# Kernel optimization log

Measured on AMD Instinct MI355X. Metric: run time of the kernel, lower is better.

## Reference

```python
import jax, jax.numpy as jnp
import numpy as np

DIM = 768; HEADS = 12; HD = DIM // HEADS; WS = 8; MLP = 4 * DIM; AH = DIM // 4
SCALE = HD ** -0.5
ADAPT_SCALE = 0.5  # self.scale in AdapterBlock3D (standard SAM-adapter constant)

def _ln(x, g, b, eps=1e-5):
    m = x.mean(-1, keepdims=True)
    v = ((x - m) ** 2).mean(-1, keepdims=True)
    return (x - m) * jax.lax.rsqrt(v + eps) * g + b

def _gelu(x):
    return jax.nn.gelu(x, approximate=False)  # torch nn.GELU default = exact erf

def _win_partition(x, ws):
    B, D, H, W, C = x.shape
    pd = (ws - D % ws) % ws; ph = (ws - H % ws) % ws; pw = (ws - W % ws) % ws
    if pd or ph or pw:
        x = jnp.pad(x, ((0, 0), (0, pd), (0, ph), (0, pw), (0, 0)))
    Dp, Hp, Wp = D + pd, H + ph, W + pw
    x = x.reshape(B, Dp // ws, ws, Hp // ws, ws, Wp // ws, ws, C)
    win = x.transpose(0, 1, 3, 5, 2, 4, 6, 7).reshape(-1, ws, ws, ws, C)
    return win, (Dp, Hp, Wp)

def _win_unpartition(win, ws, pad_dhw, dhw):
    Dp, Hp, Wp = pad_dhw; D, H, W = dhw
    B = win.shape[0] // (Dp * Hp * Wp // ws ** 3)
    x = win.reshape(B, Dp // ws, Hp // ws, Wp // ws, ws, ws, ws, -1)
    x = x.transpose(0, 1, 4, 2, 5, 3, 6, 7).reshape(B, Dp, Hp, Wp, -1)
    return x[:, :D, :H, :W, :]

def _rel(rel_pos, size):
    # q_size == k_size == size, rel_pos has 2*size-1 rows -> pure gather
    idx = jnp.arange(size)[:, None] - jnp.arange(size)[None, :] + (size - 1)
    return rel_pos[idx]  # (size, size, HD)

def _attention(x, qkv_w, qkv_b, rpd, rph, rpw, proj_w, proj_b):
    Bw = x.shape[0]; N = WS ** 3
    qkv = (x.reshape(Bw, N, DIM) @ qkv_w.T + qkv_b).reshape(Bw, N, 3, HEADS, HD)
    qkv = qkv.transpose(2, 0, 3, 1, 4).reshape(3, Bw * HEADS, N, HD)
    q, k, v = qkv[0], qkv[1], qkv[2]
    attn = jnp.einsum('bqc,bkc->bqk', q * SCALE, k)  # (Bw*H, N, N)
    rq = q.reshape(-1, WS, WS, WS, HD)
    rel_d = jnp.einsum('bdhwc,dkc->bdhwk', rq, _rel(rpd, WS))
    rel_h = jnp.einsum('bdhwc,hkc->bdhwk', rq, _rel(rph, WS))
    rel_w = jnp.einsum('bdhwc,wkc->bdhwk', rq, _rel(rpw, WS))
    attn = (attn.reshape(-1, WS, WS, WS, WS, WS, WS)
            + rel_d[:, :, :, :, :, None, None]
            + rel_h[:, :, :, :, None, :, None]
            + rel_w[:, :, :, :, None, None, :]).reshape(-1, N, N)
    attn = jax.nn.softmax(attn, axis=-1)
    out = jnp.einsum('bqk,bkc->bqc', attn, v).reshape(Bw, HEADS, WS, WS, WS, HD)
    out = out.transpose(0, 2, 3, 4, 1, 5).reshape(Bw, WS, WS, WS, DIM)
    return out @ proj_w.T + proj_b

def _adapter(x, w1, b1, w2, b2, skip):
    xs = _gelu(x @ w1.T + b1) @ w2.T + b2
    return x + xs if skip else xs

def setup_inputs() -> dict:
    key = jax.random.key(0)
    ks = jax.random.split(key, 24)
    r = lambda k, s: jax.random.normal(k, s, dtype=jnp.float32) * 0.02
    return {
        'x': jax.random.normal(ks[0], (2, 16, 16, 16, DIM), dtype=jnp.float32),
        'ln1_g': jnp.ones((DIM,), jnp.float32), 'ln1_b': jnp.zeros((DIM,), jnp.float32),
        'qkv_w': r(ks[1], (3 * DIM, DIM)), 'qkv_b': r(ks[2], (3 * DIM,)),
        'rel_pos_d': r(ks[3], (2 * WS - 1, HD)),
        'rel_pos_h': r(ks[4], (2 * WS - 1, HD)),
        'rel_pos_w': r(ks[5], (2 * WS - 1, HD)),
        'proj_w': r(ks[6], (DIM, DIM)), 'proj_b': r(ks[7], (DIM,)),
        'aa1_w': r(ks[8], (AH, DIM)), 'aa1_b': r(ks[9], (AH,)),
        'aa2_w': r(ks[10], (DIM, AH)), 'aa2_b': r(ks[11], (DIM,)),
        'ln2_g': jnp.ones((DIM,), jnp.float32), 'ln2_b': jnp.zeros((DIM,), jnp.float32),
        'mlp1_w': r(ks[12], (MLP, DIM)), 'mlp1_b': r(ks[13], (MLP,)),
        'mlp2_w': r(ks[14], (DIM, MLP)), 'mlp2_b': r(ks[15], (DIM,)),
        'ma1_w': r(ks[16], (AH, DIM)), 'ma1_b': r(ks[17], (AH,)),
        'ma2_w': r(ks[18], (DIM, AH)), 'ma2_b': r(ks[19], (DIM,)),
    }

def reference(x, ln1_g, ln1_b, qkv_w, qkv_b, rel_pos_d, rel_pos_h, rel_pos_w,
              proj_w, proj_b, aa1_w, aa1_b, aa2_w, aa2_b, ln2_g, ln2_b,
              mlp1_w, mlp1_b, mlp2_w, mlp2_b, ma1_w, ma1_b, ma2_w, ma2_b):
    B, D, H, W, C = x.shape
    shortcut = x
    h = _ln(x, ln1_g, ln1_b)
    h, pad_dhw = _win_partition(h, WS)
    h = _attention(h, qkv_w, qkv_b, rel_pos_d, rel_pos_h, rel_pos_w, proj_w, proj_b)
    h = _adapter(h, aa1_w, aa1_b, aa2_w, aa2_b, skip=True)  # Attention_Adapter
    h = _win_unpartition(h, WS, pad_dhw, (D, H, W))
    h = shortcut + h
    hn = _ln(h, ln2_g, ln2_b)
    mlp_out = _gelu(hn @ mlp1_w.T + mlp1_b) @ mlp2_w.T + mlp2_b
    adapt_out = _adapter(hn, ma1_w, ma1_b, ma2_w, ma2_b, skip=False)  # MLP_Adapter
    return h + mlp_out + ADAPT_SCALE * adapt_out
```

## Files before the change

kernel.cpp:

```cpp
#include <hip/hip_runtime.h>

typedef unsigned short u16;
typedef __attribute__((ext_vector_type(4))) float f32x4;
typedef __attribute__((ext_vector_type(8))) short s16x8;

#define TOK 8192
#define NDIM 768
#define NHEADS 12
#define WHN 192
#define WHSZ 32768
#define L2E 1.4426950408889634f
#define SCL2 (0.125f * L2E)

#if __has_builtin(__builtin_amdgcn_exp2f)
#define EXP2F __builtin_amdgcn_exp2f
#else
#define EXP2F exp2f
#endif

__device__ __forceinline__ u16 f2bf(float f) {
  union { float f; unsigned u; } x; x.f = f;
  unsigned r = x.u + 0x7fffu + ((x.u >> 16) & 1u);
  return (u16)(r >> 16);
}
__device__ __forceinline__ float bf2f(u16 u) {
  union { unsigned u; float f; } x; x.u = ((unsigned)u) << 16;
  return x.f;
}
__device__ __forceinline__ float gelu_f(float v) {
  float z = fabsf(v) * 0.70710678118654752f;
  float t = __builtin_amdgcn_rcpf(1.0f + 0.3275911f * z);
  float poly = t * (0.254829592f +
               t * (-0.284496736f +
               t * (1.421413741f +
               t * (-1.453152027f + t * 1.061405429f))));
  float erfv = 1.0f - poly * __expf(-z * z);
  erfv = copysignf(erfv, v);
  return 0.5f * v * (1.0f + erfv);
}
__device__ __forceinline__ f32x4 mfma16(s16x8 a, s16x8 b, f32x4 c) {
  return __builtin_amdgcn_mfma_f32_16x16x32_bf16(a, b, c, 0, 0, 0);
}
__device__ __forceinline__ void glds16(const u16* g, u16* l) {
  __builtin_amdgcn_global_load_lds(
      (const __attribute__((address_space(1))) unsigned int*)g,
      (__attribute__((address_space(3))) unsigned int*)l, 16, 0, 0);
}
template<int N> __device__ __forceinline__ void waitvm() {
  if constexpr (N == 0)      asm volatile("s_waitcnt vmcnt(0)" ::: "memory");
  else if constexpr (N == 2) asm volatile("s_waitcnt vmcnt(2)" ::: "memory");
  else if constexpr (N == 3) asm volatile("s_waitcnt vmcnt(3)" ::: "memory");
  else if constexpr (N == 4) asm volatile("s_waitcnt vmcnt(4)" ::: "memory");
  else if constexpr (N == 6) asm volatile("s_waitcnt vmcnt(6)" ::: "memory");
  __builtin_amdgcn_sched_barrier(0);
}
__device__ __forceinline__ int tok_of(int wi, int n) {
  int b = wi >> 3;
  int d = (((wi >> 2) & 1) << 3) | (n >> 6);
  int h = (((wi >> 1) & 1) << 3) | ((n >> 3) & 7);
  int w = ((wi & 1) << 3) | (n & 7);
  return (b << 12) | (d << 8) | (h << 4) | w;
}

struct WConv {
  const float* src[11];
  u16* dst[11];
  int n[11];
};
__global__ __launch_bounds__(256) void conv_weights(WConv a) {
  int stride = gridDim.x * blockDim.x;
  int t0 = blockIdx.x * blockDim.x + threadIdx.x;
  for (int s = 0; s < 11; s++) {
    const float4* src = (const float4*)a.src[s];
    u16* dst = a.dst[s];
    int n4 = a.n[s] >> 2;
    for (int i = t0; i < n4; i += stride) {
      float4 v = src[i];
      ushort4 o;
      o.x = f2bf(v.x); o.y = f2bf(v.y); o.z = f2bf(v.z); o.w = f2bf(v.w);
      *(ushort4*)(dst + 4 * (size_t)i) = o;
    }
  }
}

__global__ __launch_bounds__(256) void ln_bf16(const float* __restrict__ in,
    const float* __restrict__ gamma, const float* __restrict__ beta,
    u16* __restrict__ out) {
  const int row = blockIdx.x;
  const int tid = threadIdx.x;
  const float* xr = in + (size_t)row * NDIM;
  float v0 = xr[tid], v1 = xr[tid + 256], v2 = xr[tid + 512];
  float s = v0 + v1 + v2;
  float q = v0 * v0 + v1 * v1 + v2 * v2;
  for (int o = 32; o; o >>= 1) { s += __shfl_down(s, o); q += __shfl_down(q, o); }
  __shared__ float ss[4], sq[4];
  int wave = tid >> 6, lane = tid & 63;
  if (lane == 0) { ss[wave] = s; sq[wave] = q; }
  __syncthreads();
  s = ss[0] + ss[1] + ss[2] + ss[3];
  q = sq[0] + sq[1] + sq[2] + sq[3];
  float mean = s * (1.0f / 768.0f);
  float var = q * (1.0f / 768.0f) - mean * mean;
  float rstd = rsqrtf(var + 1e-5f);
  u16* orow = out + (size_t)row * NDIM;
  float v[3] = {v0, v1, v2};
  #pragma unroll
  for (int i = 0; i < 3; i++) {
    int c = tid + i * 256;
    orow[c] = f2bf((v[i] - mean) * rstd * gamma[c] + beta[c]);
  }
}

template<int BM, int BN, int TPB, int EPI>
__global__ __launch_bounds__(TPB) void gemm_bf16(
    const u16* __restrict__ A, const u16* __restrict__ W,
    const float* __restrict__ bias, int M, int N, int K,
    u16* __restrict__ obf, float* __restrict__ of,
    const float* __restrict__ add1, const float* __restrict__ add2) {
  constexpr int BK = 32;
  constexpr int WCOLS = TPB / 128;
  constexpr int WM = BM / 2, WN = BN / WCOLS;
  constexpr int MF = WM / 16, NF = WN / 16;
  constexpr int ACH = BM * BK / (8 * TPB);
  constexpr int BCH = BN * BK / (8 * TPB);
  constexpr int LPT = ACH + BCH;
  __shared__ __align__(16) u16 As[3][BM * BK];
  __shared__ __align__(16) u16 Bs[3][BN * BK];
  const int bm = blockIdx.x, bn = blockIdx.y;
  const int tid = threadIdx.x;
  const int wave = tid >> 6, lane = tid & 63;
  const int wr = wave / WCOLS, wc = wave % WCOLS;
  const int g = lane >> 4, c15 = lane & 15;
  f32x4 acc[MF][NF] = {};
  const u16* Ab = A + (size_t)(bm * BM) * K;
  const u16* Wb = W + (size_t)(bn * BN) * K;
  auto stage = [&](int k0, int b) {
    #pragma unroll
    for (int i = 0; i < ACH; i++) {
      int L = i * TPB + tid;
      glds16(Ab + (size_t)(L >> 2) * K + k0 + (((L & 3) ^ ((L >> 2) & 3)) * 8),
             &As[b][L * 8]);
    }
    #pragma unroll
    for (int i = 0; i < BCH; i++) {
      int L = i * TPB + tid;
      glds16(Wb + (size_t)(L >> 2) * K + k0 + (((L & 3) ^ ((L >> 2) & 3)) * 8),
             &Bs[b][L * 8]);
    }
  };
  const int NT = K / BK;
  stage(0, 0);
  stage(BK, 1);
  for (int t = 0; t < NT; t++) {
    int buf = t % 3;
    if (t < NT - 1) waitvm<LPT>(); else waitvm<0>();
    __builtin_amdgcn_s_barrier();
    __builtin_amdgcn_sched_barrier(0);
    if (t + 2 < NT) stage((t + 2) * BK, (t + 2) % 3);
    s16x8 af[MF], bfr[NF];
    #pragma unroll
    for (int mi = 0; mi < MF; mi++) {
      int r = wr * WM + mi * 16 + c15;
      af[mi] = *(const s16x8*)&As[buf][r * BK + ((g ^ (r & 3)) << 3)];
    }
    #pragma unroll
    for (int ni = 0; ni < NF; ni++) {
      int r = wc * WN + ni * 16 + c15;
      bfr[ni] = *(const s16x8*)&Bs[buf][r * BK + ((g ^ (r & 3)) << 3)];
    }
    __builtin_amdgcn_s_setprio(1);
    #pragma unroll
    for (int mi = 0; mi < MF; mi++)
      #pragma unroll
      for (int ni = 0; ni < NF; ni++)
        acc[mi][ni] = mfma16(af[mi], bfr[ni], acc[mi][ni]);
    __builtin_amdgcn_s_setprio(0);
  }
  #pragma unroll
  for (int mi = 0; mi < MF; mi++) {
    #pragma unroll
    for (int ni = 0; ni < NF; ni++) {
      int col = bn * BN + wc * WN + ni * 16 + c15;
      float bv = bias[col];
      #pragma unroll
      for (int j = 0; j < 4; j++) {
        int row = bm * BM + wr * WM + mi * 16 + g * 4 + j;
        size_t idx = (size_t)row * N + col;
        float v = acc[mi][ni][j] + bv;
        if (EPI == 0) {
          obf[idx] = f2bf(v);
        } else if (EPI == 1) {
          of[idx] = v; obf[idx] = f2bf(v);
        } else if (EPI == 2) {
          obf[idx] = f2bf(gelu_f(v));
        } else if (EPI == 3) {
          of[idx] = add1[idx] + add2[idx] + v;
        } else if (EPI == 4) {
          of[idx] = add1[idx] + v;
        } else if (EPI == 5) {
          of[idx] = add1[idx] + 0.5f * v;
        } else if (EPI == 6) {
          int seg = col >= 1536 ? 2 : (col >= 768 ? 1 : 0);
          int cc_ = col - seg * 768;
          int hh = cc_ >> 6, c = cc_ & 63;
          int t2 = row;
          int b = t2 >> 12, d = (t2 >> 8) & 15, hy = (t2 >> 4) & 15, wx = t2 & 15;
          int wi = (b << 3) | ((d >> 3) << 2) | ((hy >> 3) << 1) | (wx >> 3);
          int n = ((d & 7) << 6) | ((hy & 7) << 3) | (wx & 7);
          obf[(size_t)seg * (WHN * WHSZ) +
              ((size_t)(wi * NHEADS + hh) * 512 + n) * 64 + c] = f2bf(v);
        }
      }
    }
  }
}

__global__ __launch_bounds__(256) void repack_v(const u16* __restrict__ vp,
                                                u16* __restrict__ vt) {
  int whi = blockIdx.x;
  __shared__ u16 Vs[512 * 64];
  int tid = threadIdx.x;
  const u16* src = vp + (size_t)whi * WHSZ;
  for (int idx = tid; idx < 512 * 64; idx += 256) {
    int n = idx >> 6, c = idx & 63;
    Vs[(n << 6) | (c ^ (n & 63))] = src[idx];
  }
  __syncthreads();
  size_t base = (size_t)whi * WHSZ;
  #pragma unroll 1
  for (int i = 0; i < 32; i++) {
    int idx4 = tid + i * 256;
    int c = idx4 >> 7, np = (idx4 & 127) << 2;
    ushort4 o;
    o.x = Vs[((np + 0) << 6) | (c ^ ((np + 0) & 63))];
    o.y = Vs[((np + 1) << 6) | (c ^ ((np + 1) & 63))];
    o.z = Vs[((np + 2) << 6) | (c ^ ((np + 2) & 63))];
    o.w = Vs[((np + 3) << 6) | (c ^ ((np + 3) & 63))];
    *(ushort4*)(vt + base + (size_t)c * 512 + np) = o;
  }
}

__global__ __launch_bounds__(256) void attn_win(const u16* __restrict__ Qp,
    const u16* __restrict__ Kp, const u16* __restrict__ vt,
    const u16* __restrict__ rpbf, u16* __restrict__ out) {
  int blk = blockIdx.x;
  int whi = blk % WHN, qblk = blk / WHN;
  int wi = whi / NHEADS, hh = whi % NHEADS;
  int tid = threadIdx.x;
  int wave = tid >> 6, lane = tid & 63;
  int g = lane >> 4, c15 = lane & 15;
  int n0 = qblk * 128 + wave * 32;
  __shared__ __align__(16) u16 Ks[2][4096];
  __shared__ __align__(16) u16 Vs[2][4096];
  __shared__ float relf[4][32][16];
  __shared__ __align__(16) u16 pool[4][16][64];
  const u16* qbase = Qp + (size_t)whi * WHSZ;
  const u16* kbase = Kp + (size_t)whi * WHSZ;
  const u16* vbase = vt + (size_t)whi * WHSZ;

  auto stage = [&](int kc, int buf) {
    #pragma unroll
    for (int i = 0; i < 2; i++) {
      int seg = wave * 2048 + i * 1024 + lane * 16;
      int r = seg >> 7, u = (seg >> 4) & 7;
      int su = (u ^ (r & 7)) << 3;
      glds16(kbase + (size_t)(kc + r) * 64 + su, &Ks[buf][seg >> 1]);
      glds16(vbase + (size_t)r * 512 + kc + su, &Vs[buf][seg >> 1]);
    }
  };

  stage(0, 0);

  const u16* qbA = qbase + (size_t)(n0 + c15) * 64;
  const u16* qbB = qbase + (size_t)(n0 + 16 + c15) * 64;
  s16x8 aA0 = *(const s16x8*)(qbA + g * 8);
  s16x8 aA1 = *(const s16x8*)(qbA + 32 + g * 8);
  s16x8 aB0 = *(const s16x8*)(qbB + g * 8);
  s16x8 aB1 = *(const s16x8*)(qbB + 32 + g * 8);

  float* scr = (wave < 2) ? (float*)&Ks[1][0] + wave * 1024
                          : (float*)&Vs[1][0] + (wave - 2) * 1024;
  int c15c = c15 < 14 ? c15 : 14;
  #pragma unroll
  for (int ax = 0; ax < 3; ax++) {
    const u16* tb = rpbf + ax * 960 + c15c * 64;
    s16x8 b0 = *(const s16x8*)(tb + g * 8);
    s16x8 b1 = *(const s16x8*)(tb + 32 + g * 8);
    f32x4 rA = {0.f, 0.f, 0.f, 0.f}, rB = {0.f, 0.f, 0.f, 0.f};
    rA = mfma16(aA0, b0, rA); rA = mfma16(aA1, b1, rA);
    rB = mfma16(aB0, b0, rB); rB = mfma16(aB1, b1, rB);
    #pragma unroll
    for (int j = 0; j < 4; j++) {
      float vA_ = rA[j] * L2E, vB_ = rB[j] * L2E;
      if (ax == 0) {
        relf[wave][g * 4 + j][c15] = vA_;
        relf[wave][16 + g * 4 + j][c15] = vB_;
      } else {
        scr[((ax - 1) * 32 + g * 4 + j) * 16 + c15] = vA_;
        scr[((ax - 1) * 32 + 16 + g * 4 + j) * 16 + c15] = vB_;
      }
    }
  }
  asm volatile("s_waitcnt lgkmcnt(0)" ::: "memory");
  __builtin_amdgcn_sched_barrier(0);

  float rbA[4][4], rbB[4][4];
  int cdA[4], cdB[4];
  #pragma unroll
  for (int j = 0; j < 4; j++) {
    int rAi = g * 4 + j, rBi = 16 + g * 4 + j;
    int nA = n0 + rAi, nB = n0 + rBi;
    cdA[j] = (nA >> 6) + 7;
    cdB[j] = (nB >> 6) + 7;
    int kw = c15 & 7;
    float rwA = scr[(32 + rAi) * 16 + ((nA & 7) - kw + 7)];
    float rwB = scr[(32 + rBi) * 16 + ((nB & 7) - kw + 7)];
    #pragma unroll
    for (int cc = 0; cc < 4; cc++) {
      int kh = (cc * 2 + (c15 >> 3)) & 7;
      rbA[cc][j] = scr[rAi * 16 + (((nA >> 3) & 7) - kh + 7)] + rwA;
      rbB[cc][j] = scr[rBi * 16 + (((nB >> 3) & 7) - kh + 7)] + rwB;
    }
  }

  float mA = -1e30f, mB = -1e30f;
  float lA[4] = {0.f, 0.f, 0.f, 0.f}, lB[4] = {0.f, 0.f, 0.f, 0.f};
  f32x4 oA[4] = {}, oB[4] = {};

  for (int c = 0; c < 8; c++) {
    int buf = c & 1;
    waitvm<0>();
    __builtin_amdgcn_s_barrier();
    __builtin_amdgcn_sched_barrier(0);
    if (c < 7) stage((c + 1) * 64, buf ^ 1);
    f32x4 sA[4], sB[4];
    __builtin_amdgcn_s_setprio(1);
    #pragma unroll
    for (int cc = 0; cc < 4; cc++) {
      int r = cc * 16 + c15;
      const u16* kr = &Ks[buf][r * 64];
      s16x8 k0 = *(const s16x8*)(kr + ((g ^ (r & 7)) << 3));
      s16x8 k1 = *(const s16x8*)(kr + (((4 + g) ^ (r & 7)) << 3));
      f32x4 t0 = {0.f, 0.f, 0.f, 0.f};
      t0 = mfma16(aA0, k0, t0);
      sA[cc] = mfma16(aA1, k1, t0);
      f32x4 t1 = {0.f, 0.f, 0.f, 0.f};
      t1 = mfma16(aB0, k0, t1);
      sB[cc] = mfma16(aB1, k1, t1);
    }
    __builtin_amdgcn_s_setprio(0);
    float rdA[4], rdB[4];
    #pragma unroll
    for (int j = 0; j < 4; j++) {
      rdA[j] = relf[wave][g * 4 + j][cdA[j] - c];
      rdB[j] = relf[wave][16 + g * 4 + j][cdB[j] - c];
    }
    #pragma unroll
    for (int cc = 0; cc < 4; cc++)
      #pragma unroll
      for (int j = 0; j < 4; j++) {
        sA[cc][j] = sA[cc][j] * SCL2 + (rdA[j] + rbA[cc][j]);
        sB[cc][j] = sB[cc][j] * SCL2 + (rdB[j] + rbB[cc][j]);
      }
    {
      float mx = fmaxf(fmaxf(fmaxf(sA[0][0], sA[0][1]), fmaxf(sA[0][2], sA[0][3])),
                       fmaxf(fmaxf(sA[1][0], sA[1][1]), fmaxf(sA[1][2], sA[1][3])));
      mx = fmaxf(mx, fmaxf(fmaxf(fmaxf(sA[2][0], sA[2][1]), fmaxf(sA[2][2], sA[2][3])),
                           fmaxf(fmaxf(sA[3][0], sA[3][1]), fmaxf(sA[3][2], sA[3][3]))));
      #pragma unroll
      for (int msk = 1; msk < 16; msk <<= 1) mx = fmaxf(mx, __shfl_xor(mx, msk));
      if (__any(mx > mA + 8.f)) {
        float mn = fmaxf(mA, mx);
        float corr = EXP2F(mA - mn);
        #pragma unroll
        for (int j = 0; j < 4; j++) lA[j] *= corr;
        #pragma unroll
        for (int cf = 0; cf < 4; cf++)
          #pragma unroll
          for (int j = 0; j < 4; j++) oA[cf][j] *= corr;
        mA = mn;
      }
      #pragma unroll
      for (int cc = 0; cc < 4; cc++)
        #pragma unroll
        for (int j = 0; j < 4; j++) {
          float p = EXP2F(sA[cc][j] - mA);
          lA[j] += p;
          int row = g * 4 + j;
          pool[wave][row][(((cc * 2 + (c15 >> 3)) ^ (row & 7)) << 3) | (c15 & 7)] =
              f2bf(p);
        }
      asm volatile("s_waitcnt lgkmcnt(0)" ::: "memory");
      __builtin_amdgcn_sched_barrier(0);
      s16x8 pa0 = *(const s16x8*)&pool[wave][c15][(g ^ (c15 & 7)) << 3];
      s16x8 pa1 = *(const s16x8*)&pool[wave][c15][((4 + g) ^ (c15 & 7)) << 3];
      __builtin_amdgcn_s_setprio(1);
      #pragma unroll
      for (int cf = 0; cf < 4; cf++) {
        int cv = cf * 16 + c15;
        const u16* vr = &Vs[buf][cv * 64];
        oA[cf] = mfma16(pa0, *(const s16x8*)(vr + ((g ^ (cv & 7)) << 3)), oA[cf]);
        oA[cf] = mfma16(pa1, *(const s16x8*)(vr + (((4 + g) ^ (cv & 7)) << 3)), oA[cf]);
      }
      __builtin_amdgcn_s_setprio(0);
    }
    {
      float mx = fmaxf(fmaxf(fmaxf(sB[0][0], sB[0][1]), fmaxf(sB[0][2], sB[0][3])),
                       fmaxf(fmaxf(sB[1][0], sB[1][1]), fmaxf(sB[1][2], sB[1][3])));
      mx = fmaxf(mx, fmaxf(fmaxf(fmaxf(sB[2][0], sB[2][1]), fmaxf(sB[2][2], sB[2][3])),
                           fmaxf(fmaxf(sB[3][0], sB[3][1]), fmaxf(sB[3][2], sB[3][3]))));
      #pragma unroll
      for (int msk = 1; msk < 16; msk <<= 1) mx = fmaxf(mx, __shfl_xor(mx, msk));
      if (__any(mx > mB + 8.f)) {
        float mn = fmaxf(mB, mx);
        float corr = EXP2F(mB - mn);
        #pragma unroll
        for (int j = 0; j < 4; j++) lB[j] *= corr;
        #pragma unroll
        for (int cf = 0; cf < 4; cf++)
          #pragma unroll
          for (int j = 0; j < 4; j++) oB[cf][j] *= corr;
        mB = mn;
      }
      #pragma unroll
      for (int cc = 0; cc < 4; cc++)
        #pragma unroll
        for (int j = 0; j < 4; j++) {
          float p = EXP2F(sB[cc][j] - mB);
          lB[j] += p;
          int row = g * 4 + j;
          pool[wave][row][(((cc * 2 + (c15 >> 3)) ^ (row & 7)) << 3) | (c15 & 7)] =
              f2bf(p);
        }
      asm volatile("s_waitcnt lgkmcnt(0)" ::: "memory");
      __builtin_amdgcn_sched_barrier(0);
      s16x8 pa0 = *(const s16x8*)&pool[wave][c15][(g ^ (c15 & 7)) << 3];
      s16x8 pa1 = *(const s16x8*)&pool[wave][c15][((4 + g) ^ (c15 & 7)) << 3];
      __builtin_amdgcn_s_setprio(1);
      #pragma unroll
      for (int cf = 0; cf < 4; cf++) {
        int cv = cf * 16 + c15;
        const u16* vr = &Vs[buf][cv * 64];
        oB[cf] = mfma16(pa0, *(const s16x8*)(vr + ((g ^ (cv & 7)) << 3)), oB[cf]);
        oB[cf] = mfma16(pa1, *(const s16x8*)(vr + (((4 + g) ^ (cv & 7)) << 3)), oB[cf]);
      }
      __builtin_amdgcn_s_setprio(0);
    }
  }
  #pragma unroll
  for (int j = 0; j < 4; j++) {
    #pragma unroll
    for (int msk = 1; msk < 16; msk <<= 1) {
      lA[j] += __shfl_xor(lA[j], msk);
      lB[j] += __shfl_xor(lB[j], msk);
    }
    lA[j] = 1.0f / lA[j];
    lB[j] = 1.0f / lB[j];
  }
  #pragma unroll
  for (int j = 0; j < 4; j++) {
    int tA = tok_of(wi, n0 + g * 4 + j);
    int tB = tok_of(wi, n0 + 16 + g * 4 + j);
    u16* orA = out + (size_t)tA * NDIM + hh * 64;
    u16* orB = out + (size_t)tB * NDIM + hh * 64;
    #pragma unroll
    for (int cf = 0; cf < 4; cf++) {
      orA[cf * 16 + c15] = f2bf(oA[cf][j] * lA[j]);
      orB[cf * 16 + c15] = f2bf(oB[cf][j] * lB[j]);
    }
  }
}

extern "C" void kernel_launch(void* const* d_in, const int* in_sizes, int n_in,
                              void* d_out, int out_size, void* d_ws, size_t ws_size,
                              hipStream_t stream) {
  const float* x     = (const float*)d_in[0];
  const float* ln1_g = (const float*)d_in[1];
  const float* ln1_b = (const float*)d_in[2];
  const float* qkv_w = (const float*)d_in[3];
  const float* qkv_b = (const float*)d_in[4];
  const float* rpd   = (const float*)d_in[5];
  const float* rph   = (const float*)d_in[6];
  const float* rpw   = (const float*)d_in[7];
  const float* proj_w = (const float*)d_in[8];
  const float* proj_b = (const float*)d_in[9];
  const float* aa1_w = (const float*)d_in[10];
  const float* aa1_b = (const float*)d_in[11];
  const float* aa2_w = (const float*)d_in[12];
  const float* aa2_b = (const float*)d_in[13];
  const float* ln2_g = (const float*)d_in[14];
  const float* ln2_b = (const float*)d_in[15];
  const float* mlp1_w = (const float*)d_in[16];
  const float* mlp1_b = (const float*)d_in[17];
  const float* mlp2_w = (const float*)d_in[18];
  const float* mlp2_b = (const float*)d_in[19];
  const float* ma1_w = (const float*)d_in[20];
  const float* ma1_b = (const float*)d_in[21];
  const float* ma2_w = (const float*)d_in[22];
  const float* ma2_b = (const float*)d_in[23];
  float* out = (float*)d_out;
  char* ws = (char*)d_ws;

  u16* wqkv  = (u16*)(ws + 0);
  u16* wproj = (u16*)(ws + 3538944);
  u16* wmlp1 = (u16*)(ws + 4718592);
  u16* wmlp2 = (u16*)(ws + 9437184);
  u16* waa1  = (u16*)(ws + 14155776);
  u16* waa2  = (u16*)(ws + 14450688);
  u16* wma1  = (u16*)(ws + 14745600);
  u16* wma2  = (u16*)(ws + 15040512);
  u16* h1    = (u16*)(ws + 15335424);
  u16* attno = h1;
  u16* qkvp  = (u16*)(ws + 27918336);
  float* p_f = (float*)(ws + 27918336);
  u16* p_bf  = (u16*)(ws + 53084160);
  u16* vtp   = (u16*)(ws + 65667072);
  u16* hn    = vtp;
  float* h_f = (float*)(ws + 78249984);
  u16* ah    = (u16*)(ws + 103415808);
  u16* mlph  = ah;
  u16* mah   = (u16*)(ws + 153747456);
  u16* rpbf  = (u16*)(ws + 153747456);
  (void)ws_size; (void)in_sizes; (void)n_in; (void)out_size;

  u16* Qp = qkvp;
  u16* Kp = qkvp + (size_t)WHN * WHSZ;
  u16* Vp = qkvp + 2 * (size_t)WHN * WHSZ;

  WConv wc;
  wc.src[0] = qkv_w;  wc.dst[0] = wqkv;  wc.n[0] = 2304 * 768;
  wc.src[1] = proj_w; wc.dst[1] = wproj; wc.n[1] = 768 * 768;
  wc.src[2] = mlp1_w; wc.dst[2] = wmlp1; wc.n[2] = 3072 * 768;
  wc.src[3] = mlp2_w; wc.dst[3] = wmlp2; wc.n[3] = 768 * 3072;
  wc.src[4] = aa1_w;  wc.dst[4] = waa1;  wc.n[4] = 192 * 768;
  wc.src[5] = aa2_w;  wc.dst[5] = waa2;  wc.n[5] = 768 * 192;
  wc.src[6] = ma1_w;  wc.dst[6] = wma1;  wc.n[6] = 192 * 768;
  wc.src[7] = ma2_w;  wc.dst[7] = wma2;  wc.n[7] = 768 * 192;
  wc.src[8] = rpd;    wc.dst[8] = rpbf;  wc.n[8] = 15 * 64;
  wc.src[9] = rph;    wc.dst[9] = rpbf + 960;  wc.n[9] = 15 * 64;
  wc.src[10] = rpw;   wc.dst[10] = rpbf + 1920; wc.n[10] = 15 * 64;
  conv_weights<<<1024, 256, 0, stream>>>(wc);

  ln_bf16<<<TOK, 256, 0, stream>>>(x, ln1_g, ln1_b, h1);
  gemm_bf16<128, 128, 512, 6><<<dim3(64, 18), 512, 0, stream>>>(
      h1, wqkv, qkv_b, TOK, 2304, 768, qkvp, nullptr, nullptr, nullptr);
  repack_v<<<192, 256, 0, stream>>>(Vp, vtp);
  attn_win<<<768, 256, 0, stream>>>(Qp, Kp, vtp, rpbf, attno);
  gemm_bf16<128, 64, 256, 1><<<dim3(64, 12), 256, 0, stream>>>(
      attno, wproj, proj_b, TOK, 768, 768, p_bf, p_f, nullptr, nullptr);
  gemm_bf16<64, 64, 256, 2><<<dim3(128, 3), 256, 0, stream>>>(
      p_bf, waa1, aa1_b, TOK, 192, 768, ah, nullptr, nullptr, nullptr);
  gemm_bf16<128, 64, 256, 3><<<dim3(64, 12), 256, 0, stream>>>(
      ah, waa2, aa2_b, TOK, 768, 192, nullptr, h_f, x, p_f);
  ln_bf16<<<TOK, 256, 0, stream>>>(h_f, ln2_g, ln2_b, hn);
  gemm_bf16<128, 128, 512, 2><<<dim3(64, 24), 512, 0, stream>>>(
      hn, wmlp1, mlp1_b, TOK, 3072, 768, mlph, nullptr, nullptr, nullptr);
  gemm_bf16<128, 64, 256, 4><<<dim3(64, 12), 256, 0, stream>>>(
      mlph, wmlp2, mlp2_b, TOK, 768, 3072, nullptr, out, h_f, nullptr);
  gemm_bf16<64, 64, 256, 2><<<dim3(128, 3), 256, 0, stream>>>(
      hn, wma1, ma1_b, TOK, 192, 768, mah, nullptr, nullptr, nullptr);
  gemm_bf16<128, 64, 256, 5><<<dim3(64, 12), 256, 0, stream>>>(
      mah, wma2, ma2_b, TOK, 768, 192, nullptr, out, out, nullptr);
}
```

Measured before the change: 323.1 us.

## Fuse MLP-adapter GEMM into MLP2 via dual K-loop and deepen GEMM pipeline

The second MLP GEMM now runs a second K-loop over the MLP-adapter hidden and its up-projection weights, which are pre-scaled by 0.5 during weight conversion. This removes a separate GEMM launch and an extra fp32 read-modify-write of the output. The projection GEMM now writes only a bf16 result, which the adapter-residual epilogue reads back in place of an fp32 copy. That cuts fp32 traffic but adds bf16 rounding to the residual path. Most 256-thread GEMMs move to a 4-buffer LDS pipeline with prefetch depth 3, which uses more shared memory and may lower occupancy.

After: 309.5 us. 4.2% less time.

```diff
diff --git a/kernel.cpp b/kernel.cpp
--- a/kernel.cpp
+++ b/kernel.cpp
@@ -66,6 +66,7 @@
   const float* src[11];
   u16* dst[11];
   int n[11];
+  float scl[11];
 };
 __global__ __launch_bounds__(256) void conv_weights(WConv a) {
   int stride = gridDim.x * blockDim.x;
@@ -73,11 +74,13 @@
   for (int s = 0; s < 11; s++) {
     const float4* src = (const float4*)a.src[s];
     u16* dst = a.dst[s];
+    float sc = a.scl[s];
     int n4 = a.n[s] >> 2;
     for (int i = t0; i < n4; i += stride) {
       float4 v = src[i];
       ushort4 o;
-      o.x = f2bf(v.x); o.y = f2bf(v.y); o.z = f2bf(v.z); o.w = f2bf(v.w);
+      o.x = f2bf(v.x * sc); o.y = f2bf(v.y * sc);
+      o.z = f2bf(v.z * sc); o.w = f2bf(v.w * sc);
       *(ushort4*)(dst + 4 * (size_t)i) = o;
     }
   }
@@ -111,12 +114,14 @@
   }
 }
 
-template<int BM, int BN, int TPB, int EPI>
+template<int BM, int BN, int TPB, int NBUF, int EPI>
 __global__ __launch_bounds__(TPB) void gemm_bf16(
     const u16* __restrict__ A, const u16* __restrict__ W,
     const float* __restrict__ bias, int M, int N, int K,
     u16* __restrict__ obf, float* __restrict__ of,
-    const float* __restrict__ add1, const float* __restrict__ add2) {
+    const float* __restrict__ add1,
+    const u16* __restrict__ A2, const u16* __restrict__ W2, int K2,
+    const float* __restrict__ bias2) {
   constexpr int BK = 32;
   constexpr int WCOLS = TPB / 128;
   constexpr int WM = BM / 2, WN = BN / WCOLS;
@@ -124,64 +129,78 @@
   constexpr int ACH = BM * BK / (8 * TPB);
   constexpr int BCH = BN * BK / (8 * TPB);
   constexpr int LPT = ACH + BCH;
-  __shared__ __align__(16) u16 As[3][BM * BK];
-  __shared__ __align__(16) u16 Bs[3][BN * BK];
+  __shared__ __align__(16) u16 As[NBUF][BM * BK];
+  __shared__ __align__(16) u16 Bs[NBUF][BN * BK];
   const int bm = blockIdx.x, bn = blockIdx.y;
   const int tid = threadIdx.x;
   const int wave = tid >> 6, lane = tid & 63;
   const int wr = wave / WCOLS, wc = wave % WCOLS;
   const int g = lane >> 4, c15 = lane & 15;
   f32x4 acc[MF][NF] = {};
-  const u16* Ab = A + (size_t)(bm * BM) * K;
-  const u16* Wb = W + (size_t)(bn * BN) * K;
-  auto stage = [&](int k0, int b) {
+  auto stage = [&](const u16* Ab_, const u16* Wb_, int Kst, int k0, int b) {
     #pragma unroll
     for (int i = 0; i < ACH; i++) {
       int L = i * TPB + tid;
-      glds16(Ab + (size_t)(L >> 2) * K + k0 + (((L & 3) ^ ((L >> 2) & 3)) * 8),
+      glds16(Ab_ + (size_t)(L >> 2) * Kst + k0 + (((L & 3) ^ ((L >> 2) & 3)) * 8),
              &As[b][L * 8]);
     }
     #pragma unroll
     for (int i = 0; i < BCH; i++) {
       int L = i * TPB + tid;
-      glds16(Wb + (size_t)(L >> 2) * K + k0 + (((L & 3) ^ ((L >> 2) & 3)) * 8),
+      glds16(Wb_ + (size_t)(L >> 2) * Kst + k0 + (((L & 3) ^ ((L >> 2) & 3)) * 8),
              &Bs[b][L * 8]);
     }
   };
-  const int NT = K / BK;
-  stage(0, 0);
-  stage(BK, 1);
-  for (int t = 0; t < NT; t++) {
-    int buf = t % 3;
-    if (t < NT - 1) waitvm<LPT>(); else waitvm<0>();
+  auto gloop = [&](const u16* Ap, const u16* Wp, int Kst) {
+    const u16* Ab_ = Ap + (size_t)(bm * BM) * Kst;
+    const u16* Wb_ = Wp + (size_t)(bn * BN) * Kst;
+    const int NT = Kst / BK;
+    asm volatile("s_waitcnt lgkmcnt(0)" ::: "memory");
     __builtin_amdgcn_s_barrier();
     __builtin_amdgcn_sched_barrier(0);
-    if (t + 2 < NT) stage((t + 2) * BK, (t + 2) % 3);
-    s16x8 af[MF], bfr[NF];
-    #pragma unroll
-    for (int mi = 0; mi < MF; mi++) {
-      int r = wr * WM + mi * 16 + c15;
-      af[mi] = *(const s16x8*)&As[buf][r * BK + ((g ^ (r & 3)) << 3)];
-    }
-    #pragma unroll
-    for (int ni = 0; ni < NF; ni++) {
-      int r = wc * WN + ni * 16 + c15;
-      bfr[ni] = *(const s16x8*)&Bs[buf][r * BK + ((g ^ (r & 3)) << 3)];
-    }
-    __builtin_amdgcn_s_setprio(1);
-    #pragma unroll
-    for (int mi = 0; mi < MF; mi++)
-      #pragma unroll
-      for (int ni = 0; ni < NF; ni++)
-        acc[mi][ni] = mfma16(af[mi], bfr[ni], acc[mi][ni]);
-    __builtin_amdgcn_s_setprio(0);
-  }
+    for (int p = 0; p < NBUF - 1 && p < NT; p++) stage(Ab_, Wb_, Kst, p * BK, p);
+    for (int t = 0; t < NT; t++) {
+      int buf = t % NBUF;
+      if constexpr (NBUF == 4) {
+        if (t + 2 < NT) waitvm<2 * LPT>();
+        else if (t + 1 < NT) waitvm<LPT>();
+        else waitvm<0>();
+      } else {
+        if (t + 1 < NT) waitvm<LPT>(); else waitvm<0>();
+      }
+      __builtin_amdgcn_s_barrier();
+      __builtin_amdgcn_sched_barrier(0);
+      if (t + NBUF - 1 < NT) stage(Ab_, Wb_, Kst, (t + NBUF - 1) * BK,
+                                   (t + NBUF - 1) % NBUF);
+      s16x8 af[MF], bfr[NF];
+      #pragma unroll
+      for (int mi = 0; mi < MF; mi++) {
+        int r = wr * WM + mi * 16 + c15;
+        af[mi] = *(const s16x8*)&As[buf][r * BK + ((g ^ (r & 3)) << 3)];
+      }
+      #pragma unroll
+      for (int ni = 0; ni < NF; ni++) {
+        int r = wc * WN + ni * 16 + c15;
+        bfr[ni] = *(const s16x8*)&Bs[buf][r * BK + ((g ^ (r & 3)) << 3)];
+      }
+      __builtin_amdgcn_s_setprio(1);
+      #pragma unroll
+      for (int mi = 0; mi < MF; mi++)
+        #pragma unroll
+        for (int ni = 0; ni < NF; ni++)
+          acc[mi][ni] = mfma16(af[mi], bfr[ni], acc[mi][ni]);
+      __builtin_amdgcn_s_setprio(0);
+    }
+  };
+  gloop(A, W, K);
+  if constexpr (EPI == 7) gloop(A2, W2, K2);
   #pragma unroll
   for (int mi = 0; mi < MF; mi++) {
     #pragma unroll
     for (int ni = 0; ni < NF; ni++) {
       int col = bn * BN + wc * WN + ni * 16 + c15;
       float bv = bias[col];
+      if (EPI == 7) bv += 0.5f * bias2[col];
       #pragma unroll
       for (int j = 0; j < 4; j++) {
         int row = bm * BM + wr * WM + mi * 16 + g * 4 + j;
@@ -189,16 +208,12 @@
         float v = acc[mi][ni][j] + bv;
         if (EPI == 0) {
           obf[idx] = f2bf(v);
-        } else if (EPI == 1) {
-          of[idx] = v; obf[idx] = f2bf(v);
         } else if (EPI == 2) {
           obf[idx] = f2bf(gelu_f(v));
         } else if (EPI == 3) {
-          of[idx] = add1[idx] + add2[idx] + v;
-        } else if (EPI == 4) {
+          of[idx] = add1[idx] + bf2f(obf[idx]) + v;
+        } else if (EPI == 7) {
           of[idx] = add1[idx] + v;
-        } else if (EPI == 5) {
-          of[idx] = add1[idx] + 0.5f * v;
         } else if (EPI == 6) {
           int seg = col >= 1536 ? 2 : (col >= 768 ? 1 : 0);
           int cc_ = col - seg * 768;
@@ -512,7 +527,6 @@
   u16* h1    = (u16*)(ws + 15335424);
   u16* attno = h1;
   u16* qkvp  = (u16*)(ws + 27918336);
-  float* p_f = (float*)(ws + 27918336);
   u16* p_bf  = (u16*)(ws + 53084160);
   u16* vtp   = (u16*)(ws + 65667072);
   u16* hn    = vtp;
@@ -528,6 +542,7 @@
   u16* Vp = qkvp + 2 * (size_t)WHN * WHSZ;
 
   WConv wc;
+  for (int i = 0; i < 11; i++) wc.scl[i] = 1.0f;
   wc.src[0] = qkv_w;  wc.dst[0] = wqkv;  wc.n[0] = 2304 * 768;
   wc.src[1] = proj_w; wc.dst[1] = wproj; wc.n[1] = 768 * 768;
   wc.src[2] = mlp1_w; wc.dst[2] = wmlp1; wc.n[2] = 3072 * 768;
@@ -536,29 +551,35 @@
   wc.src[5] = aa2_w;  wc.dst[5] = waa2;  wc.n[5] = 768 * 192;
   wc.src[6] = ma1_w;  wc.dst[6] = wma1;  wc.n[6] = 192 * 768;
   wc.src[7] = ma2_w;  wc.dst[7] = wma2;  wc.n[7] = 768 * 192;
+  wc.scl[7] = 0.5f;
   wc.src[8] = rpd;    wc.dst[8] = rpbf;  wc.n[8] = 15 * 64;
   wc.src[9] = rph;    wc.dst[9] = rpbf + 960;  wc.n[9] = 15 * 64;
   wc.src[10] = rpw;   wc.dst[10] = rpbf + 1920; wc.n[10] = 15 * 64;
   conv_weights<<<1024, 256, 0, stream>>>(wc);
 
   ln_bf16<<<TOK, 256, 0, stream>>>(x, ln1_g, ln1_b, h1);
-  gemm_bf16<128, 128, 512, 6><<<dim3(64, 18), 512, 0, stream>>>(
-      h1, wqkv, qkv_b, TOK, 2304, 768, qkvp, nullptr, nullptr, nullptr);
+  gemm_bf16<128, 128, 512, 3, 6><<<dim3(64, 18), 512, 0, stream>>>(
+      h1, wqkv, qkv_b, TOK, 2304, 768, qkvp, nullptr, nullptr,
+      nullptr, nullptr, 0, nullptr);
   repack_v<<<192, 256, 0, stream>>>(Vp, vtp);
   attn_win<<<768, 256, 0, stream>>>(Qp, Kp, vtp, rpbf, attno);
-  gemm_bf16<128, 64, 256, 1><<<dim3(64, 12), 256, 0, stream>>>(
-      attno, wproj, proj_b, TOK, 768, 768, p_bf, p_f, nullptr, nullptr);
-  gemm_bf16<64, 64, 256, 2><<<dim3(128, 3), 256, 0, stream>>>(
-      p_bf, waa1, aa1_b, TOK, 192, 768, ah, nullptr, nullptr, nullptr);
-  gemm_bf16<128, 64, 256, 3><<<dim3(64, 12), 256, 0, stream>>>(
-      ah, waa2, aa2_b, TOK, 768, 192, nullptr, h_f, x, p_f);
+  gemm_bf16<128, 64, 256, 4, 0><<<dim3(64, 12), 256, 0, stream>>>(
+      attno, wproj, proj_b, TOK, 768, 768, p_bf, nullptr, nullptr,
+      nullptr, nullptr, 0, nullptr);
+  gemm_bf16<64, 64, 256, 4, 2><<<dim3(128, 3), 256, 0, stream>>>(
+      p_bf, waa1, aa1_b, TOK, 192, 768, ah, nullptr, nullptr,
+      nullptr, nullptr, 0, nullptr);
+  gemm_bf16<128, 64, 256, 4, 3><<<dim3(64, 12), 256, 0, stream>>>(
+      ah, waa2, aa2_b, TOK, 768, 192, p_bf, h_f, x,
+      nullptr, nullptr, 0, nullptr);
   ln_bf16<<<TOK, 256, 0, stream>>>(h_f, ln2_g, ln2_b, hn);
-  gemm_bf16<128, 128, 512, 2><<<dim3(64, 24), 512, 0, stream>>>(
-      hn, wmlp1, mlp1_b, TOK, 3072, 768, mlph, nullptr, nullptr, nullptr);
-  gemm_bf16<128, 64, 256, 4><<<dim3(64, 12), 256, 0, stream>>>(
-      mlph, wmlp2, mlp2_b, TOK, 768, 3072, nullptr, out, h_f, nullptr);
-  gemm_bf16<64, 64, 256, 2><<<dim3(128, 3), 256, 0, stream>>>(
-      hn, wma1, ma1_b, TOK, 192, 768, mah, nullptr, nullptr, nullptr);
-  gemm_bf16<128, 64, 256, 5><<<dim3(64, 12), 256, 0, stream>>>(
-      mah, wma2, ma2_b, TOK, 768, 192, nullptr, out, out, nullptr);
-}
+  gemm_bf16<64, 64, 256, 4, 2><<<dim3(128, 3), 256, 0, stream>>>(
+      hn, wma1, ma1_b, TOK, 192, 768, mah, nullptr, nullptr,
+      nullptr, nullptr, 0, nullptr);
+  gemm_bf16<128, 128, 512, 3, 2><<<dim3(64, 24), 512, 0, stream>>>(
+      hn, wmlp1, mlp1_b, TOK, 3072, 768, mlph, nullptr, nullptr,
+      nullptr, nullptr, 0, nullptr);
+  gemm_bf16<128, 64, 256, 4, 7><<<dim3(64, 12), 256, 0, stream>>>(
+      mlph, wmlp2, mlp2_b, TOK, 768, 3072, nullptr, out, h_f,
+      mah, wma2, 192, ma2_b);
+}
```
